# Kernel optimization log

Hardware: AMD Instinct MI355X
Metric: run time of the kernel (lower is better)

## Reference

```python
import jax, jax.numpy as jnp
import numpy as np

N, XD, NF, HH, WW = 32, 3, 160, 32, 32
KD, VD = 16, NF // 2            # K=16, V=80
CK, CQ = XD * 3 + NF, XD * 2 + NF  # 169, 166


def concat_elu(x):
    # axis = ndim-3 == channel axis for NCHW
    return jax.nn.elu(jnp.concatenate([x, -x], axis=1))


def nin(x, W, b):
    # 1x1 conv / channel-wise linear: W [out, in], x [n, in, h, w]
    return jnp.einsum('oc,nchw->nohw', W, x) + b[None, :, None, None]


def grn(x, Wi, bi, Wo, bo, a=None, Ws=None, bs=None):
    h = nin(concat_elu(x), Wi, bi)
    if a is not None:
        h = h + nin(concat_elu(a), Ws, bs)
    h = concat_elu(h)  # Dropout2d is identity at inference
    h = nin(h, Wo, bo)
    ga, gb = jnp.split(h, 2, axis=1)
    return x + ga * jax.nn.sigmoid(gb)


def causal_softmax(s, eps=1e-7):
    hw = s.shape[-1]
    mask = jnp.tril(jnp.ones((hw, hw), dtype=bool), -1)  # strictly lower triangular
    s = jnp.where(mask, s, 0.0)               # torch.tril(x, -1): zeros, NOT -inf (faithful)
    w = jax.nn.softmax(s, axis=-1)            # softmax over full row incl. the zeros
    w = jnp.where(mask, w, 0.0)               # re-mask
    return w / (jnp.sum(w, axis=-1, keepdims=True) + eps)  # renormalize


def reference(x, ul, b, gkWi, gkbi, gkWo, gkbo, gqWi, gqbi, gqWo, gqbo, gvWi, gvbi, gvWo, gvbo, nkW, nkb, nqW, nqb, nvW, nvb, goWi, gobi, goWs, gobs, goWo, gobo):
    n, _, h, w = x.shape
    hw = h * w
    ul_b = jnp.concatenate([ul, b], axis=1)      # [n, 166, h, w]
    x_ul_b = jnp.concatenate([x, ul_b], axis=1)  # [n, 169, h, w]
    keys = nin(grn(x_ul_b, gkWi, gkbi, gkWo, gkbo), nkW, nkb).reshape(n, KD, hw)
    queries = nin(grn(ul_b, gqWi, gqbi, gqWo, gqbo), nqW, nqb).reshape(n, KD, hw)
    values = nin(grn(x_ul_b, gvWi, gvbi, gvWo, gvbo), nvW, nvb).reshape(n, VD, hw)
    presoftmax = jnp.einsum('nji,njk->nki', keys, queries)  # [n, hw_q, hw_k]
    att_w = causal_softmax(presoftmax)
    att_v = jnp.einsum('nij,nkj->nki', att_w, values).reshape(n, VD, h, w)
    return grn(ul, goWi, gobi, goWo, gobo, a=att_v, Ws=goWs, bs=gobs)


def setup_inputs():
    key = jax.random.key(0)
    keys = iter(jax.random.split(key, 32))
    def rn(shape, s=1.0):
        return jax.random.normal(next(keys), shape, dtype=jnp.float32) * s
    z = lambda c: jnp.zeros((c,), jnp.float32)
    return dict(
        x=rn((N, XD, HH, WW)), ul=rn((N, NF, HH, WW)), b=rn((N, 2 * XD, HH, WW)),
        gkWi=rn((CK, 2 * CK), 0.05), gkbi=z(CK), gkWo=rn((2 * CK, 2 * CK), 0.05), gkbo=z(2 * CK),
        gqWi=rn((CQ, 2 * CQ), 0.05), gqbi=z(CQ), gqWo=rn((2 * CQ, 2 * CQ), 0.05), gqbo=z(2 * CQ),
        gvWi=rn((CK, 2 * CK), 0.05), gvbi=z(CK), gvWo=rn((2 * CK, 2 * CK), 0.05), gvbo=z(2 * CK),
        nkW=rn((KD, CK), 0.05), nkb=z(KD), nqW=rn((KD, CQ), 0.05), nqb=z(KD),
        nvW=rn((VD, CK), 0.05), nvb=z(VD),
        goWi=rn((NF, 2 * NF), 0.05), gobi=z(NF), goWs=rn((NF, NF), 0.05), gobs=z(NF),
        goWo=rn((2 * NF, 2 * NF), 0.05), gobo=z(2 * NF),
    )
```

## Files before the change

kernel.cpp:

```cpp
#include <hip/hip_runtime.h>
#include <cstddef>
#include <cstdint>

#define HW 1024
#define NBATCH 32

typedef unsigned short ushort_t;
typedef unsigned int uint_t;
typedef short s16x8 __attribute__((ext_vector_type(8)));
typedef float f32x4 __attribute__((ext_vector_type(4)));
typedef float f32x16 __attribute__((ext_vector_type(16)));
typedef unsigned int u32x4 __attribute__((ext_vector_type(4)));

__device__ __forceinline__ float elu1(float z){ return z > 0.f ? z : __expf(z) - 1.f; }
__device__ __forceinline__ float sigm(float z){ return 1.f/(1.f+__expf(-z)); }
__device__ __forceinline__ ushort_t f2bf(float f){
  uint_t u = __builtin_bit_cast(uint_t, f);
  u += 0x7FFFu + ((u >> 16) & 1u);
  return (ushort_t)(u >> 16);
}
__device__ __forceinline__ float bf2f(ushort_t h){
  uint_t u = ((uint_t)h) << 16;
  return __builtin_bit_cast(float, u);
}
__device__ __forceinline__ uint_t cvtpk(float lo, float hi){
  uint_t r;
  asm("v_cvt_pk_bf16_f32 %0, %1, %2" : "=v"(r) : "v"(lo), "v"(hi));
  return r;
}
__device__ __forceinline__ void gload_lds16(const void* g, void* l){
  __builtin_amdgcn_global_load_lds((const __attribute__((address_space(1))) unsigned int*)g,
                                   (__attribute__((address_space(3))) unsigned int*)l, 16, 0, 0);
}

__device__ __forceinline__ const float* src_ptr(const float* x, const float* ul, const float* b,
                                                int n, int c, int gm){
  if (gm == 0){
    if (c < 3)   return x  + ((size_t)n*3   + c)*HW;
    if (c < 163) return ul + ((size_t)n*160 + (c-3))*HW;
    return b + ((size_t)n*6 + (c-163))*HW;
  } else if (gm == 1){
    if (c < 160) return ul + ((size_t)n*160 + c)*HW;
    return b + ((size_t)n*6 + (c-160))*HW;
  }
  return ul + ((size_t)n*160 + c)*HW;
}

template<int GM>
__global__ void k_act(const float* __restrict__ x, const float* __restrict__ ul,
                      const float* __restrict__ b, const float* __restrict__ av,
                      ushort_t* __restrict__ out, int Cb, int P1, int CP){
  int pxg = blockIdx.x*256 + threadIdx.x;
  int n = pxg >> 10, hw = pxg & 1023;
  int c8 = blockIdx.y*8;
  ushort_t* orow = out + (size_t)pxg * CP;
  ushort_t pbuf[8], nbuf[8];
  #pragma unroll
  for (int j = 0; j < 8; ++j){
    int c = c8 + j;
    float s = 0.f;
    if (c < Cb){
      if (GM == 3) s = av[((size_t)(n*80 + c))*HW + hw];
      else         s = src_ptr(x, ul, b, n, c, GM)[hw];
    }
    pbuf[j] = f2bf(elu1(s));
    nbuf[j] = f2bf(elu1(-s));
  }
  uint4 up, un;
  up.x = (uint_t)pbuf[0] | ((uint_t)pbuf[1]<<16);
  up.y = (uint_t)pbuf[2] | ((uint_t)pbuf[3]<<16);
  up.z = (uint_t)pbuf[4] | ((uint_t)pbuf[5]<<16);
  up.w = (uint_t)pbuf[6] | ((uint_t)pbuf[7]<<16);
  un.x = (uint_t)nbuf[0] | ((uint_t)nbuf[1]<<16);
  un.y = (uint_t)nbuf[2] | ((uint_t)nbuf[3]<<16);
  un.z = (uint_t)nbuf[4] | ((uint_t)nbuf[5]<<16);
  un.w = (uint_t)nbuf[6] | ((uint_t)nbuf[7]<<16);
  *(uint4*)(orow + c8)      = up;
  *(uint4*)(orow + P1 + c8) = un;
}

struct SPtrs { const float* p[12]; };
struct WCfg  { int dst[12], O[12], Kt[12], K1[12], P1[12], Opad[12], Kpad[12], Oh[12]; };

__global__ void k_wconv(SPtrs sp, WCfg c, ushort_t* __restrict__ Wb){
  int d = blockIdx.y;
  const float* src = sp.p[d];
  int O = c.O[d], Kt = c.Kt[d], K1 = c.K1[d], P1 = c.P1[d], Op = c.Opad[d], Kp = c.Kpad[d], Oh = c.Oh[d];
  ushort_t* dst = Wb + c.dst[d];
  int total = Op*Kp, K2 = Kt - K1;
  for (int i = blockIdx.x*256 + threadIdx.x; i < total; i += 32*256){
    int o = i / Kp, kk = i - o*Kp;
    int k = (kk < K1) ? kk : ((kk >= P1 && kk < P1 + K2) ? (K1 + kk - P1) : -1);
    int so; bool rv;
    if (Oh > 0){
      if (o < 192){ so = o; rv = (o < Oh); }
      else        { so = Oh + (o - 192); rv = ((o - 192) < Oh); }
    } else { so = o; rv = (o < O); }
    float v = (rv && k >= 0) ? src[(size_t)so*Kt + k] : 0.f;
    dst[i] = f2bf(v);
  }
}

template<int EPI>
__global__ __launch_bounds__(256) void k_gmm2(const ushort_t* __restrict__ Wb, const float* __restrict__ bias,
    const ushort_t* __restrict__ act, const float* __restrict__ accin, void* __restrict__ outv,
    const float* __restrict__ xp, const float* __restrict__ ulp, const float* __restrict__ bp,
    int O, int Kpad, int CP, int OP, int P1o, int AST)
{
  __shared__ ushort_t Blds[4][2][2048];
  const int tid = threadIdx.x;
  const int w = tid >> 6, l = tid & 63;
  const int n = blockIdx.x >> 2, hw0 = (blockIdx.x & 3)*256;
  const bool FUSED = (EPI >= 5);
  const int o0 = blockIdx.y*(FUSED ? 32 : 64);

  const ushort_t* actw = act + (size_t)(n*HW + hw0 + w*64)*CP;
  const ushort_t* Wbo  = Wb + (size_t)o0*Kpad;
  const size_t r2off = FUSED ? (size_t)192*Kpad : (size_t)32*Kpad;

#define STAGE2(bufi, ktv) do { \
    int cl_ = (l & 3) ^ ((l >> 4) & 2); \
    _Pragma("unroll") \
    for (int s_ = 0; s_ < 4; ++s_){ \
      const ushort_t* g_ = actw + (size_t)(s_*16 + (l>>2))*CP + (ktv)*32 + cl_*8; \
      gload_lds16(g_, &Blds[w][bufi][s_*512]); \
    } \
  } while(0)

  f32x4 acc[4][4];
  #pragma unroll
  for (int i = 0; i < 4; ++i)
    #pragma unroll
    for (int j = 0; j < 4; ++j) acc[i][j] = (f32x4){0.f,0.f,0.f,0.f};

  const int NT = Kpad >> 5;
  STAGE2(0, 0);
  for (int kt = 0; kt < NT; ++kt){
    int cur = kt & 1;
    const ushort_t* Ab = Wbo + (size_t)(l&15)*Kpad + kt*32 + (l>>4)*8;
    s16x8 a0 = *(const s16x8*)(Ab);
    s16x8 a1 = *(const s16x8*)(Ab + 16*Kpad);
    s16x8 a2 = *(const s16x8*)(Ab + r2off);
    s16x8 a3 = *(const s16x8*)(Ab + r2off + 16*Kpad);
    if (kt + 1 < NT) STAGE2(cur^1, kt+1);
    asm volatile("s_waitcnt vmcnt(4)" ::: "memory");
    const ushort_t* Bb = &Blds[w][cur][0];
    const int chp = ((l>>4) ^ ((l>>2)&2))*8;
    #pragma unroll
    for (int po = 0; po < 4; ++po){
      s16x8 bv = *(const s16x8*)(Bb + po*512 + (l&15)*32 + chp);
      acc[po][0] = __builtin_amdgcn_mfma_f32_16x16x32_bf16(a0, bv, acc[po][0], 0, 0, 0);
      acc[po][1] = __builtin_amdgcn_mfma_f32_16x16x32_bf16(a1, bv, acc[po][1], 0, 0, 0);
      acc[po][2] = __builtin_amdgcn_mfma_f32_16x16x32_bf16(a2, bv, acc[po][2], 0, 0, 0);
      acc[po][3] = __builtin_amdgcn_mfma_f32_16x16x32_bf16(a3, bv, acc[po][3], 0, 0, 0);
    }
  }
#undef STAGE2

  const int g = l >> 4, cc = l & 15;

  if (FUSED){
    const int gm = P1o;
    #pragma unroll
    for (int oo = 0; oo < 2; ++oo){
      int ch = o0 + oo*16 + g*4;
      #pragma unroll
      for (int po = 0; po < 4; ++po){
        int px = hw0 + w*64 + po*16 + cc;
        size_t pb = (size_t)n*HW + px;
        float rr[4];
        #pragma unroll
        for (int i = 0; i < 4; ++i){
          int c = ch + i;
          float r = 0.f;
          if (c < O){
            float ga = acc[po][oo][i]   + bias[c];
            float gb = acc[po][oo+2][i] + bias[O + c];
            float s  = src_ptr(xp, ulp, bp, n, c, gm)[px];
            r = s + ga*sigm(gb);
          }
          rr[i] = r;
        }
        if (EPI == 5){
          uint2 pk;
          pk.x = (uint_t)f2bf(rr[0]) | ((uint_t)f2bf(rr[1])<<16);
          pk.y = (uint_t)f2bf(rr[2]) | ((uint_t)f2bf(rr[3])<<16);
          *(uint2*)((ushort_t*)outv + pb*OP + ch) = pk;
        } else {
          #pragma unroll
          for (int i = 0; i < 4; ++i)
            if (ch + i < O) ((float*)outv)[((size_t)n*O + ch + i)*HW + px] = rr[i];
        }
      }
    }
    return;
  }

  #pragma unroll
  for (int oo = 0; oo < 4; ++oo){
    int ch = o0 + oo*16 + g*4;
    if (ch >= O) continue;
    float b0 = bias[ch];
    float b1 = (ch+1 < O) ? bias[ch+1] : 0.f;
    float b2 = (ch+2 < O) ? bias[ch+2] : 0.f;
    float b3 = (ch+3 < O) ? bias[ch+3] : 0.f;
    #pragma unroll
    for (int po = 0; po < 4; ++po){
      int px = hw0 + w*64 + po*16 + cc;
      size_t pb = (size_t)n*HW + px;
      f32x4 a = acc[po][oo];
      float h0 = a[0]+b0, h1 = a[1]+b1, h2v = a[2]+b2, h3 = a[3]+b3;
      if (EPI == 3){
        float4 av4 = *(const float4*)(accin + pb*AST + ch);
        h0 += av4.x; h1 += av4.y; h2v += av4.z; h3 += av4.w;
      }
      if (EPI == 0){
        *(float4*)((float*)outv + pb*OP + ch) = make_float4(h0, h1, h2v, h3);
      } else if (EPI == 1){
        uint2 pk;
        pk.x = (uint_t)f2bf(h0)  | ((uint_t)f2bf(h1)<<16);
        pk.y = (uint_t)f2bf(h2v) | ((uint_t)f2bf(h3)<<16);
        *(uint2*)((ushort_t*)outv + pb*OP + ch) = pk;
      } else if (EPI == 2 || EPI == 3){
        ushort_t* op = (ushort_t*)outv + pb*OP;
        uint2 pp, pn;
        pp.x = (uint_t)f2bf(elu1(h0))  | ((uint_t)f2bf(elu1(h1))<<16);
        pp.y = (uint_t)f2bf(elu1(h2v)) | ((uint_t)f2bf(elu1(h3))<<16);
        pn.x = (uint_t)f2bf(elu1(-h0))  | ((uint_t)f2bf(elu1(-h1))<<16);
        pn.y = (uint_t)f2bf(elu1(-h2v)) | ((uint_t)f2bf(elu1(-h3))<<16);
        *(uint2*)(op + ch) = pp;
        *(uint2*)(op + P1o + ch) = pn;
      } else {
        ushort_t* ob = (ushort_t*)outv;
        float hv[4] = {h0, h1, h2v, h3};
        #pragma unroll
        for (int i = 0; i < 4; ++i)
          if (ch + i < O) ob[((size_t)n*OP + ch + i)*HW + px] = f2bf(hv[i]);
      }
    }
  }
}

__global__ __launch_bounds__(64) void k_attn2(const ushort_t* __restrict__ Kp,
    const ushort_t* __restrict__ Qp, const ushort_t* __restrict__ Vc, float* __restrict__ AV){
  const int l = threadIdx.x;
  const int qt = blockIdx.x, n = blockIdx.y;
  const int hi = l >> 5, qcol = l & 31;
  const int qg = qt*32 + qcol;

  s16x8 bq = *(const s16x8*)(Qp + ((size_t)(n*HW + qg))*16 + hi*8);

  f32x16 acc0, acc1, acc2;
  #pragma unroll
  for (int r = 0; r < 16; ++r){ acc0[r]=0.f; acc1[r]=0.f; acc2[r]=0.f; }
  float m = 0.f, S = 0.f;
  const int nkt = qt + 1;

  for (int kt = 0; kt < nkt; ++kt){
    const int j0 = kt*32;
    s16x8 ak = *(const s16x8*)(Kp + ((size_t)(n*HW + j0 + qcol))*16 + hi*8);
    f32x16 zc;
    #pragma unroll
    for (int r = 0; r < 16; ++r) zc[r] = 0.f;
    f32x16 p = __builtin_amdgcn_mfma_f32_32x32x16_bf16(ak, bq, zc, 0, 0, 0);

    float ps[16];
    float tmax = -3.0e38f;
    const bool diag = (kt == qt);
    #pragma unroll
    for (int r = 0; r < 16; ++r){
      int kk = j0 + (r&3) + 8*(r>>2) + 4*hi;
      float sv = p[r];
      if (diag && kk >= qg) sv = -3.0e38f;
      ps[r] = sv;
      tmax = fmaxf(tmax, sv);
    }
    tmax = fmaxf(tmax, __shfl_xor(tmax, 32));
    if (tmax > m + 8.f){
      float f = __expf(m - tmax);
      S *= f;
      #pragma unroll
      for (int r = 0; r < 16; ++r){ acc0[r]*=f; acc1[r]*=f; acc2[r]*=f; }
      m = tmax;
    }
    float pe[16], ts = 0.f;
    #pragma unroll
    for (int r = 0; r < 16; ++r){ pe[r] = __expf(ps[r] - m); ts += pe[r]; }
    S += ts + __shfl_xor(ts, 32);

    uint_t w0 = cvtpk(pe[0],  pe[1]),  w1 = cvtpk(pe[2],  pe[3]);
    uint_t w2 = cvtpk(pe[4],  pe[5]),  w3 = cvtpk(pe[6],  pe[7]);
    uint_t w4 = cvtpk(pe[8],  pe[9]),  w5 = cvtpk(pe[10], pe[11]);
    uint_t w6 = cvtpk(pe[12], pe[13]), w7 = cvtpk(pe[14], pe[15]);
    uint_t o0 = __shfl_xor((int)w0, 32), o1 = __shfl_xor((int)w1, 32);
    uint_t o2 = __shfl_xor((int)w2, 32), o3 = __shfl_xor((int)w3, 32);
    uint_t o4 = __shfl_xor((int)w4, 32), o5 = __shfl_xor((int)w5, 32);
    uint_t o6 = __shfl_xor((int)w6, 32), o7 = __shfl_xor((int)w7, 32);
    u32x4 f0, f1;
    f0.x = hi ? o2 : w0; f0.y = hi ? o3 : w1; f0.z = hi ? w2 : o0; f0.w = hi ? w3 : o1;
    f1.x = hi ? o6 : w4; f1.y = hi ? o7 : w5; f1.z = hi ? w6 : o4; f1.w = hi ? w7 : o5;
    s16x8 pb0 = __builtin_bit_cast(s16x8, f0);
    s16x8 pb1 = __builtin_bit_cast(s16x8, f1);

    const ushort_t* vb = Vc + ((size_t)(n*96 + qcol))*HW + j0 + hi*8;
    s16x8 v00 = *(const s16x8*)(vb);
    s16x8 v01 = *(const s16x8*)(vb + 16);
    s16x8 v10 = *(const s16x8*)(vb + 32*HW);
    s16x8 v11 = *(const s16x8*)(vb + 32*HW + 16);
    s16x8 v20 = *(const s16x8*)(vb + 64*HW);
    s16x8 v21 = *(const s16x8*)(vb + 64*HW + 16);
    acc0 = __builtin_amdgcn_mfma_f32_32x32x16_bf16(v00, pb0, acc0, 0, 0, 0);
    acc0 = __builtin_amdgcn_mfma_f32_32x32x16_bf16(v01, pb1, acc0, 0, 0, 0);
    acc1 = __builtin_amdgcn_mfma_f32_32x32x16_bf16(v10, pb0, acc1, 0, 0, 0);
    acc1 = __builtin_amdgcn_mfma_f32_32x32x16_bf16(v11, pb1, acc1, 0, 0, 0);
    acc2 = __builtin_amdgcn_mfma_f32_32x32x16_bf16(v20, pb0, acc2, 0, 0, 0);
    acc2 = __builtin_amdgcn_mfma_f32_32x32x16_bf16(v21, pb1, acc2, 0, 0, 0);
  }

  float Z = S + (float)(HW - qg)*__expf(-m);
  float inv = 1.f/(S + 1e-7f*Z);
  #pragma unroll
  for (int r = 0; r < 16; ++r){
    int vr = (r&3) + 8*(r>>2) + 4*hi;
    AV[((size_t)(n*80 + vr))*HW + qg]      = acc0[r]*inv;
    AV[((size_t)(n*80 + 32 + vr))*HW + qg] = acc1[r]*inv;
    if (64 + vr < 80) AV[((size_t)(n*80 + 64 + vr))*HW + qg] = acc2[r]*inv;
  }
}

extern "C" void kernel_launch(void* const* d_in, const int* in_sizes, int n_in,
                              void* d_out, int out_size, void* d_ws, size_t ws_size,
                              hipStream_t stream) {
  const float* x    = (const float*)d_in[0];
  const float* ul   = (const float*)d_in[1];
  const float* bb   = (const float*)d_in[2];
  const float* gkWi = (const float*)d_in[3];  const float* gkbi = (const float*)d_in[4];
  const float* gkWo = (const float*)d_in[5];  const float* gkbo = (const float*)d_in[6];
  const float* gqWi = (const float*)d_in[7];  const float* gqbi = (const float*)d_in[8];
  const float* gqWo = (const float*)d_in[9];  const float* gqbo = (const float*)d_in[10];
  const float* gvWi = (const float*)d_in[11]; const float* gvbi = (const float*)d_in[12];
  const float* gvWo = (const float*)d_in[13]; const float* gvbo = (const float*)d_in[14];
  const float* nkW  = (const float*)d_in[15]; const float* nkb  = (const float*)d_in[16];
  const float* nqW  = (const float*)d_in[17]; const float* nqb  = (const float*)d_in[18];
  const float* nvW  = (const float*)d_in[19]; const float* nvb  = (const float*)d_in[20];
  const float* goWi = (const float*)d_in[21]; const float* gobi = (const float*)d_in[22];
  const float* goWs = (const float*)d_in[23]; const float* gobs = (const float*)d_in[24];
  const float* goWo = (const float*)d_in[25]; const float* gobo = (const float*)d_in[26];
  float* outp = (float*)d_out;
  char* wsb = (char*)d_ws;

  ushort_t* R0 = (ushort_t*)(wsb + 0);
  ushort_t* R1 = (ushort_t*)(wsb + 23068672);
  ushort_t* R2 = (ushort_t*)(wsb + 46137344);
  ushort_t* R3 = (ushort_t*)(wsb + 71303168);
  ushort_t* Kp = (ushort_t*)(wsb + 83886080);
  ushort_t* Qp = (ushort_t*)(wsb + 84934656);
  ushort_t* Vc = (ushort_t*)(wsb + 85983232);
  float*    AV = (float*)   (wsb + 92274688);
  ushort_t* Wb = (ushort_t*)(wsb + 102760448);

  static const int dDst[12]  = {0,67584,202752,215040,282624,417792,430080,497664,632832,657408,718848,749568};
  static const int dO[12]    = {169,338,16,166,332,16,169,338,80,160,160,320};
  static const int dKt[12]   = {338,338,169,332,332,166,338,338,169,320,160,320};
  static const int dK1[12]   = {169,169,169,166,166,166,169,169,169,160,80,320};
  static const int dP1[12]   = {176,176,9999,176,176,9999,176,176,9999,160,80,9999};
  static const int dOp[12]   = {192,384,64,192,384,64,192,384,128,192,192,384};
  static const int dKp[12]   = {352,352,192,352,352,192,352,352,192,320,160,320};
  static const int dOh[12]   = {0,169,0,0,166,0,0,169,0,0,0,160};

  SPtrs sp; WCfg wc;
  const float* srcs[12] = {gkWi,gkWo,nkW,gqWi,gqWo,nqW,gvWi,gvWo,nvW,goWi,goWs,goWo};
  for (int i = 0; i < 12; ++i){
    sp.p[i] = srcs[i];
    wc.dst[i]=dDst[i]; wc.O[i]=dO[i]; wc.Kt[i]=dKt[i]; wc.K1[i]=dK1[i];
    wc.P1[i]=dP1[i]; wc.Opad[i]=dOp[i]; wc.Kpad[i]=dKp[i]; wc.Oh[i]=dOh[i];
  }

  dim3 b256(256), b64t(64);
  k_wconv<<<dim3(32,12), b256, 0, stream>>>(sp, wc, Wb);

#define GMM2(EPI, DI, GY, BIASP, ACT, ACCIN, OUT, O_, CP_, OP_, P1O_, AST_) \
  k_gmm2<EPI><<<dim3(128, GY), b256, 0, stream>>>( \
    Wb + dDst[DI], BIASP, (const ushort_t*)(ACT), ACCIN, OUT, x, ul, bb, \
    O_, dKp[DI], CP_, OP_, P1O_, AST_)

  k_act<0><<<dim3(128,22), b256, 0, stream>>>(x, ul, bb, nullptr, R0, 169, 176, 352);
  GMM2(2, 0, 3, gkbi, R0, nullptr, R1, 169, 352, 352, 176, 0);
  GMM2(5, 1, 6, gkbo, R1, nullptr, R3, 169, 352, 192, 0, 0);
  GMM2(1, 2, 1, nkb, R3, nullptr, Kp, 16, 192, 16, 0, 0);

  GMM2(2, 6, 3, gvbi, R0, nullptr, R1, 169, 352, 352, 176, 0);
  GMM2(5, 7, 6, gvbo, R1, nullptr, R3, 169, 352, 192, 0, 0);
  GMM2(4, 8, 2, nvb, R3, nullptr, Vc, 80, 192, 96, 0, 0);

  k_act<1><<<dim3(128,22), b256, 0, stream>>>(x, ul, bb, nullptr, R0, 166, 176, 352);
  GMM2(2, 3, 3, gqbi, R0, nullptr, R1, 166, 352, 352, 176, 0);
  GMM2(5, 4, 6, gqbo, R1, nullptr, R3, 166, 352, 192, 1, 0);
  GMM2(1, 5, 1, nqb, R3, nullptr, Qp, 16, 192, 16, 0, 0);

  k_attn2<<<dim3(32, 32), b64t, 0, stream>>>(Kp, Qp, Vc, AV);

  k_act<2><<<dim3(128,20), b256, 0, stream>>>(x, ul, bb, nullptr, R1, 160, 160, 320);
  k_act<3><<<dim3(128,10), b256, 0, stream>>>(x, ul, bb, AV, R3, 80, 80, 160);
  GMM2(0, 9, 3, gobi, R1, nullptr, (float*)R0, 160, 320, 160, 0, 0);
  GMM2(3, 10, 3, gobs, R3, (const float*)R0, R2, 160, 160, 320, 160, 160);
  GMM2(6, 11, 5, gobo, R2, nullptr, outp, 160, 320, 0, 2, 0);
}
```

Before: 474.0 us.

## Fuse key/value input GEMMs, attention concat-ELU epilogue, and output GEMM concatenation

The key and value first-layer GEMMs now run as one launch over a shared activation buffer, with a split epilogue that writes two outputs. The attention kernel applies concat-ELU itself and writes bf16 directly into a combined 480-wide activation buffer next to the ul concat-ELU. The output block's Wi and Ws GEMMs are merged into a single K=480 GEMM with summed biases, using concatenated weights. This removes the fp32 AV round trip, one k_act launch, and the fp32 intermediate accumulation pass, at the cost of a wider GEMM and more epilogue work in attention.

```diff
diff --git a/kernel.cpp b/kernel.cpp
--- a/kernel.cpp
+++ b/kernel.cpp
@@ -48,7 +48,7 @@
 
 template<int GM>
 __global__ void k_act(const float* __restrict__ x, const float* __restrict__ ul,
-                      const float* __restrict__ b, const float* __restrict__ av,
+                      const float* __restrict__ b,
                       ushort_t* __restrict__ out, int Cb, int P1, int CP){
   int pxg = blockIdx.x*256 + threadIdx.x;
   int n = pxg >> 10, hw = pxg & 1023;
@@ -59,10 +59,7 @@
   for (int j = 0; j < 8; ++j){
     int c = c8 + j;
     float s = 0.f;
-    if (c < Cb){
-      if (GM == 3) s = av[((size_t)(n*80 + c))*HW + hw];
-      else         s = src_ptr(x, ul, b, n, c, GM)[hw];
-    }
+    if (c < Cb) s = src_ptr(x, ul, b, n, c, GM)[hw];
     pbuf[j] = f2bf(elu1(s));
     nbuf[j] = f2bf(elu1(-s));
   }
@@ -84,10 +81,22 @@
 
 __global__ void k_wconv(SPtrs sp, WCfg c, ushort_t* __restrict__ Wb){
   int d = blockIdx.y;
-  const float* src = sp.p[d];
   int O = c.O[d], Kt = c.Kt[d], K1 = c.K1[d], P1 = c.P1[d], Op = c.Opad[d], Kp = c.Kpad[d], Oh = c.Oh[d];
   ushort_t* dst = Wb + c.dst[d];
-  int total = Op*Kp, K2 = Kt - K1;
+  int total = Op*Kp;
+  if (d == 9){
+    const float* wi = sp.p[9];
+    const float* ws = sp.p[11];
+    for (int i = blockIdx.x*256 + threadIdx.x; i < total; i += 32*256){
+      int o = i / Kp, kk = i - o*Kp;
+      float v = 0.f;
+      if (o < O) v = (kk < 320) ? wi[(size_t)o*320 + kk] : ws[(size_t)o*160 + (kk - 320)];
+      dst[i] = f2bf(v);
+    }
+    return;
+  }
+  const float* src = sp.p[d];
+  int K2 = Kt - K1;
   for (int i = blockIdx.x*256 + threadIdx.x; i < total; i += 32*256){
     int o = i / Kp, kk = i - o*Kp;
     int k = (kk < K1) ? kk : ((kk >= P1 && kk < P1 + K2) ? (K1 + kk - P1) : -1);
@@ -102,16 +111,17 @@
 }
 
 template<int EPI>
-__global__ __launch_bounds__(256) void k_gmm2(const ushort_t* __restrict__ Wb, const float* __restrict__ bias,
-    const ushort_t* __restrict__ act, const float* __restrict__ accin, void* __restrict__ outv,
+__global__ __launch_bounds__(256) void k_gmm2(const ushort_t* __restrict__ Wb,
+    const float* __restrict__ bias, const float* __restrict__ bias2,
+    const ushort_t* __restrict__ act, void* __restrict__ outv, void* __restrict__ outv2,
     const float* __restrict__ xp, const float* __restrict__ ulp, const float* __restrict__ bp,
-    int O, int Kpad, int CP, int OP, int P1o, int AST)
+    int O, int Kpad, int CP, int OP, int P1o)
 {
   __shared__ ushort_t Blds[4][2][2048];
   const int tid = threadIdx.x;
   const int w = tid >> 6, l = tid & 63;
   const int n = blockIdx.x >> 2, hw0 = (blockIdx.x & 3)*256;
-  const bool FUSED = (EPI >= 5);
+  const bool FUSED = (EPI == 5 || EPI == 6);
   const int o0 = blockIdx.y*(FUSED ? 32 : 64);
 
   const ushort_t* actw = act + (size_t)(n*HW + hw0 + w*64)*CP;
@@ -199,50 +209,53 @@
   #pragma unroll
   for (int oo = 0; oo < 4; ++oo){
     int ch = o0 + oo*16 + g*4;
-    if (ch >= O) continue;
-    float b0 = bias[ch];
-    float b1 = (ch+1 < O) ? bias[ch+1] : 0.f;
-    float b2 = (ch+2 < O) ? bias[ch+2] : 0.f;
-    float b3 = (ch+3 < O) ? bias[ch+3] : 0.f;
+    int c = ch;
+    const float* bsp = bias;
+    ushort_t* oP = (ushort_t*)outv;
+    if (EPI == 8 && ch >= 192){ c = ch - 192; bsp = bias2; oP = (ushort_t*)outv2; }
+    if (c >= O) continue;
+    float b0 = bsp[c];
+    float b1 = (c+1 < O) ? bsp[c+1] : 0.f;
+    float b2 = (c+2 < O) ? bsp[c+2] : 0.f;
+    float b3 = (c+3 < O) ? bsp[c+3] : 0.f;
+    if (EPI == 7){
+      b0 += bias2[c];
+      if (c+1 < O) b1 += bias2[c+1];
+      if (c+2 < O) b2 += bias2[c+2];
+      if (c+3 < O) b3 += bias2[c+3];
+    }
     #pragma unroll
     for (int po = 0; po < 4; ++po){
       int px = hw0 + w*64 + po*16 + cc;
       size_t pb = (size_t)n*HW + px;
       f32x4 a = acc[po][oo];
       float h0 = a[0]+b0, h1 = a[1]+b1, h2v = a[2]+b2, h3 = a[3]+b3;
-      if (EPI == 3){
-        float4 av4 = *(const float4*)(accin + pb*AST + ch);
-        h0 += av4.x; h1 += av4.y; h2v += av4.z; h3 += av4.w;
-      }
-      if (EPI == 0){
-        *(float4*)((float*)outv + pb*OP + ch) = make_float4(h0, h1, h2v, h3);
-      } else if (EPI == 1){
+      if (EPI == 1){
         uint2 pk;
         pk.x = (uint_t)f2bf(h0)  | ((uint_t)f2bf(h1)<<16);
         pk.y = (uint_t)f2bf(h2v) | ((uint_t)f2bf(h3)<<16);
-        *(uint2*)((ushort_t*)outv + pb*OP + ch) = pk;
-      } else if (EPI == 2 || EPI == 3){
-        ushort_t* op = (ushort_t*)outv + pb*OP;
+        *(uint2*)(oP + pb*OP + c) = pk;
+      } else if (EPI == 2 || EPI == 7 || EPI == 8){
+        ushort_t* op = oP + pb*OP;
         uint2 pp, pn;
         pp.x = (uint_t)f2bf(elu1(h0))  | ((uint_t)f2bf(elu1(h1))<<16);
         pp.y = (uint_t)f2bf(elu1(h2v)) | ((uint_t)f2bf(elu1(h3))<<16);
         pn.x = (uint_t)f2bf(elu1(-h0))  | ((uint_t)f2bf(elu1(-h1))<<16);
         pn.y = (uint_t)f2bf(elu1(-h2v)) | ((uint_t)f2bf(elu1(-h3))<<16);
-        *(uint2*)(op + ch) = pp;
-        *(uint2*)(op + P1o + ch) = pn;
+        *(uint2*)(op + c) = pp;
+        *(uint2*)(op + P1o + c) = pn;
       } else {
-        ushort_t* ob = (ushort_t*)outv;
         float hv[4] = {h0, h1, h2v, h3};
         #pragma unroll
         for (int i = 0; i < 4; ++i)
-          if (ch + i < O) ob[((size_t)n*OP + ch + i)*HW + px] = f2bf(hv[i]);
+          if (c + i < O) oP[((size_t)n*OP + c + i)*HW + px] = f2bf(hv[i]);
       }
     }
   }
 }
 
 __global__ __launch_bounds__(64) void k_attn2(const ushort_t* __restrict__ Kp,
-    const ushort_t* __restrict__ Qp, const ushort_t* __restrict__ Vc, float* __restrict__ AV){
+    const ushort_t* __restrict__ Qp, const ushort_t* __restrict__ Vc, ushort_t* __restrict__ Mb){
   const int l = threadIdx.x;
   const int qt = blockIdx.x, n = blockIdx.y;
   const int hi = l >> 5, qcol = l & 31;
@@ -319,12 +332,37 @@
 
   float Z = S + (float)(HW - qg)*__expf(-m);
   float inv = 1.f/(S + 1e-7f*Z);
+  ushort_t* mrow = Mb + (size_t)(n*HW + qg)*480 + 320;
   #pragma unroll
-  for (int r = 0; r < 16; ++r){
-    int vr = (r&3) + 8*(r>>2) + 4*hi;
-    AV[((size_t)(n*80 + vr))*HW + qg]      = acc0[r]*inv;
-    AV[((size_t)(n*80 + 32 + vr))*HW + qg] = acc1[r]*inv;
-    if (64 + vr < 80) AV[((size_t)(n*80 + 64 + vr))*HW + qg] = acc2[r]*inv;
+  for (int rg = 0; rg < 4; ++rg){
+    int vb = 8*rg + 4*hi;
+    float a0v[4], a1v[4];
+    #pragma unroll
+    for (int i = 0; i < 4; ++i){ a0v[i] = acc0[4*rg+i]*inv; a1v[i] = acc1[4*rg+i]*inv; }
+    uint2 pp, pn;
+    pp.x = (uint_t)f2bf(elu1(a0v[0]))  | ((uint_t)f2bf(elu1(a0v[1]))<<16);
+    pp.y = (uint_t)f2bf(elu1(a0v[2]))  | ((uint_t)f2bf(elu1(a0v[3]))<<16);
+    pn.x = (uint_t)f2bf(elu1(-a0v[0])) | ((uint_t)f2bf(elu1(-a0v[1]))<<16);
+    pn.y = (uint_t)f2bf(elu1(-a0v[2])) | ((uint_t)f2bf(elu1(-a0v[3]))<<16);
+    *(uint2*)(mrow + vb) = pp;
+    *(uint2*)(mrow + 80 + vb) = pn;
+    pp.x = (uint_t)f2bf(elu1(a1v[0]))  | ((uint_t)f2bf(elu1(a1v[1]))<<16);
+    pp.y = (uint_t)f2bf(elu1(a1v[2]))  | ((uint_t)f2bf(elu1(a1v[3]))<<16);
+    pn.x = (uint_t)f2bf(elu1(-a1v[0])) | ((uint_t)f2bf(elu1(-a1v[1]))<<16);
+    pn.y = (uint_t)f2bf(elu1(-a1v[2])) | ((uint_t)f2bf(elu1(-a1v[3]))<<16);
+    *(uint2*)(mrow + 32 + vb) = pp;
+    *(uint2*)(mrow + 112 + vb) = pn;
+    if (rg < 2){
+      float a2v[4];
+      #pragma unroll
+      for (int i = 0; i < 4; ++i) a2v[i] = acc2[4*rg+i]*inv;
+      pp.x = (uint_t)f2bf(elu1(a2v[0]))  | ((uint_t)f2bf(elu1(a2v[1]))<<16);
+      pp.y = (uint_t)f2bf(elu1(a2v[2]))  | ((uint_t)f2bf(elu1(a2v[3]))<<16);
+      pn.x = (uint_t)f2bf(elu1(-a2v[0])) | ((uint_t)f2bf(elu1(-a2v[1]))<<16);
+      pn.y = (uint_t)f2bf(elu1(-a2v[2])) | ((uint_t)f2bf(elu1(-a2v[3]))<<16);
+      *(uint2*)(mrow + 64 + vb) = pp;
+      *(uint2*)(mrow + 144 + vb) = pn;
+    }
   }
 }
 
@@ -349,27 +387,28 @@
   float* outp = (float*)d_out;
   char* wsb = (char*)d_ws;
 
-  ushort_t* R0 = (ushort_t*)(wsb + 0);
-  ushort_t* R1 = (ushort_t*)(wsb + 23068672);
-  ushort_t* R2 = (ushort_t*)(wsb + 46137344);
-  ushort_t* R3 = (ushort_t*)(wsb + 71303168);
-  ushort_t* Kp = (ushort_t*)(wsb + 83886080);
-  ushort_t* Qp = (ushort_t*)(wsb + 84934656);
-  ushort_t* Vc = (ushort_t*)(wsb + 85983232);
-  float*    AV = (float*)   (wsb + 92274688);
-  ushort_t* Wb = (ushort_t*)(wsb + 102760448);
-
-  static const int dDst[12]  = {0,67584,202752,215040,282624,417792,430080,497664,632832,657408,718848,749568};
-  static const int dO[12]    = {169,338,16,166,332,16,169,338,80,160,160,320};
-  static const int dKt[12]   = {338,338,169,332,332,166,338,338,169,320,160,320};
-  static const int dK1[12]   = {169,169,169,166,166,166,169,169,169,160,80,320};
-  static const int dP1[12]   = {176,176,9999,176,176,9999,176,176,9999,160,80,9999};
-  static const int dOp[12]   = {192,384,64,192,384,64,192,384,128,192,192,384};
-  static const int dKp[12]   = {352,352,192,352,352,192,352,352,192,320,160,320};
-  static const int dOh[12]   = {0,169,0,0,166,0,0,169,0,0,0,160};
+  ushort_t* R0  = (ushort_t*)(wsb + 0);
+  ushort_t* R1k = (ushort_t*)(wsb + 23068672);
+  ushort_t* R1v = (ushort_t*)(wsb + 46137344);
+  ushort_t* R3  = (ushort_t*)(wsb + 69206016);
+  ushort_t* Kp  = (ushort_t*)(wsb + 81788928);
+  ushort_t* Qp  = (ushort_t*)(wsb + 82837504);
+  ushort_t* Vc  = (ushort_t*)(wsb + 83886080);
+  ushort_t* M   = (ushort_t*)(wsb + 90177536);
+  ushort_t* R2  = (ushort_t*)(wsb + 121634816);
+  ushort_t* Wb  = (ushort_t*)(wsb + 142606336);
+
+  static const int dDst[12] = {0,67584,135168,270336,405504,417792,442368,509952,645120,657408,749568,0};
+  static const int dO[12]   = {169,169,338,338,16,80,166,332,16,160,320,0};
+  static const int dKt[12]  = {338,338,338,338,169,169,332,332,166,0,320,0};
+  static const int dK1[12]  = {169,169,169,169,169,169,166,166,166,0,320,0};
+  static const int dP1[12]  = {176,176,176,176,9999,9999,176,176,9999,0,9999,0};
+  static const int dOp[12]  = {192,192,384,384,64,128,192,384,64,192,384,0};
+  static const int dKp[12]  = {352,352,352,352,192,192,352,352,192,480,320,0};
+  static const int dOh[12]  = {0,0,169,169,0,0,0,166,0,0,160,0};
 
   SPtrs sp; WCfg wc;
-  const float* srcs[12] = {gkWi,gkWo,nkW,gqWi,gqWo,nqW,gvWi,gvWo,nvW,goWi,goWs,goWo};
+  const float* srcs[12] = {gkWi,gvWi,gkWo,gvWo,nkW,nvW,gqWi,gqWo,nqW,goWi,goWo,goWs};
   for (int i = 0; i < 12; ++i){
     sp.p[i] = srcs[i];
     wc.dst[i]=dDst[i]; wc.O[i]=dO[i]; wc.Kt[i]=dKt[i]; wc.K1[i]=dK1[i];
@@ -377,32 +416,29 @@
   }
 
   dim3 b256(256), b64t(64);
-  k_wconv<<<dim3(32,12), b256, 0, stream>>>(sp, wc, Wb);
-
-#define GMM2(EPI, DI, GY, BIASP, ACT, ACCIN, OUT, O_, CP_, OP_, P1O_, AST_) \
+  k_wconv<<<dim3(32,11), b256, 0, stream>>>(sp, wc, Wb);
+
+#define GMM2(EPI, DI, GY, B1, B2, ACT, OUT, OUT2, O_, CP_, OP_, P1O_) \
   k_gmm2<EPI><<<dim3(128, GY), b256, 0, stream>>>( \
-    Wb + dDst[DI], BIASP, (const ushort_t*)(ACT), ACCIN, OUT, x, ul, bb, \
-    O_, dKp[DI], CP_, OP_, P1O_, AST_)
-
-  k_act<0><<<dim3(128,22), b256, 0, stream>>>(x, ul, bb, nullptr, R0, 169, 176, 352);
-  GMM2(2, 0, 3, gkbi, R0, nullptr, R1, 169, 352, 352, 176, 0);
-  GMM2(5, 1, 6, gkbo, R1, nullptr, R3, 169, 352, 192, 0, 0);
-  GMM2(1, 2, 1, nkb, R3, nullptr, Kp, 16, 192, 16, 0, 0);
-
-  GMM2(2, 6, 3, gvbi, R0, nullptr, R1, 169, 352, 352, 176, 0);
-  GMM2(5, 7, 6, gvbo, R1, nullptr, R3, 169, 352, 192, 0, 0);
-  GMM2(4, 8, 2, nvb, R3, nullptr, Vc, 80, 192, 96, 0, 0);
-
-  k_act<1><<<dim3(128,22), b256, 0, stream>>>(x, ul, bb, nullptr, R0, 166, 176, 352);
-  GMM2(2, 3, 3, gqbi, R0, nullptr, R1, 166, 352, 352, 176, 0);
-  GMM2(5, 4, 6, gqbo, R1, nullptr, R3, 166, 352, 192, 1, 0);
-  GMM2(1, 5, 1, nqb, R3, nullptr, Qp, 16, 192, 16, 0, 0);
-
-  k_attn2<<<dim3(32, 32), b64t, 0, stream>>>(Kp, Qp, Vc, AV);
-
-  k_act<2><<<dim3(128,20), b256, 0, stream>>>(x, ul, bb, nullptr, R1, 160, 160, 320);
-  k_act<3><<<dim3(128,10), b256, 0, stream>>>(x, ul, bb, AV, R3, 80, 80, 160);
-  GMM2(0, 9, 3, gobi, R1, nullptr, (float*)R0, 160, 320, 160, 0, 0);
-  GMM2(3, 10, 3, gobs, R3, (const float*)R0, R2, 160, 160, 320, 160, 160);
-  GMM2(6, 11, 5, gobo, R2, nullptr, outp, 160, 320, 0, 2, 0);
-}
+    Wb + dDst[DI], B1, B2, (const ushort_t*)(ACT), OUT, OUT2, x, ul, bb, \
+    O_, dKp[DI], CP_, OP_, P1O_)
+
+  k_act<0><<<dim3(128,22), b256, 0, stream>>>(x, ul, bb, R0, 169, 176, 352);
+  GMM2(8, 0, 6, gkbi, gvbi, R0, R1k, R1v, 169, 352, 352, 176);
+  GMM2(5, 2, 6, gkbo, nullptr, R1k, R3, nullptr, 169, 352, 192, 0);
+  GMM2(1, 4, 1, nkb, nullptr, R3, Kp, nullptr, 16, 192, 16, 0);
+  GMM2(5, 3, 6, gvbo, nullptr, R1v, R3, nullptr, 169, 352, 192, 0);
+  GMM2(4, 5, 2, nvb, nullptr, R3, Vc, nullptr, 80, 192, 96, 0);
+
+  k_act<1><<<dim3(128,22), b256, 0, stream>>>(x, ul, bb, R0, 166, 176, 352);
+  GMM2(2, 6, 3, gqbi, nullptr, R0, R1k, nullptr, 166, 352, 352, 176);
+  GMM2(5, 7, 6, gqbo, nullptr, R1k, R3, nullptr, 166, 352, 192, 1);
+  GMM2(1, 8, 1, nqb, nullptr, R3, Qp, nullptr, 16, 192, 16, 0);
+
+  k_act<2><<<dim3(128,20), b256, 0, stream>>>(x, ul, bb, M, 160, 160, 480);
+
+  k_attn2<<<dim3(32, 32), b64t, 0, stream>>>(Kp, Qp, Vc, M);
+
+  GMM2(7, 9, 3, gobi, gobs, M, R2, nullptr, 160, 480, 320, 160);
+  GMM2(6, 10, 5, gobo, nullptr, R2, outp, nullptr, 160, 320, 0, 2);
+}
```

Result: faster. 445.2 us (-6.1%).
